# Kernel tuning notes

Hardware: AMD Instinct MI355X
Metric: run time of the kernel (lower is better)

## Reference

```python
import jax, jax.numpy as jnp
import numpy as np

NEG_INF = -1.0e9  # matches torch masked_fill value

def setup_inputs() -> dict:
    key = jax.random.key(0)
    kq, kk, kv, km = jax.random.split(key, 4)
    B, S, D = 16, 2048, 128
    query = jax.random.normal(kq, (B, S, D), dtype=jnp.float32)
    k = jax.random.normal(kk, (B, S, D), dtype=jnp.float32)
    value = jax.random.normal(kv, (B, S, D), dtype=jnp.float32)
    mask = jax.random.randint(km, (B, S, S), 0, 2).astype(jnp.bool_)
    return {"query": query, "key": k, "value": value, "mask": mask}

def reference(query, key, value, mask):
    # scores: [B, Sq, Sk]
    D = key.shape[-1]
    scale = jnp.sqrt(jnp.asarray(D, dtype=query.dtype))
    scores = jnp.einsum('bqd,bkd->bqk', query, key) / scale
    scores = jnp.where(mask, jnp.asarray(NEG_INF, dtype=scores.dtype), scores)
    attn = jax.nn.softmax(scores, axis=2)
    # dropout p=0.0 -> identity in eval/reference
    out = jnp.einsum('bqk,bkd->bqd', attn, value)
    return out, attn
```

## Files before the change

kernel.cpp:

```cpp
#include <hip/hip_runtime.h>

#define S 2048
#define Dh 128
#define NB 16
#define OUT_ELEMS ((size_t)NB * S * Dh)
#define NEG_BIG -1.0e9f
#define SCALE 0.08838834764831845f

typedef __attribute__((ext_vector_type(8))) short bf16x8;
typedef __attribute__((ext_vector_type(4))) float f32x4;
typedef __attribute__((ext_vector_type(4))) short s16x4;

__device__ __forceinline__ short f2bf(float x) {
    unsigned u = __float_as_uint(x);
    u += 0x7fffu + ((u >> 16) & 1u);
    return (short)(u >> 16);
}

__device__ __forceinline__ s16x4 pack4(float4 v) {
    s16x4 r;
    r.x = f2bf(v.x); r.y = f2bf(v.y); r.z = f2bf(v.z); r.w = f2bf(v.w);
    return r;
}

__global__ void detect_mask(const unsigned char* __restrict__ m, int* __restrict__ flag) {
    __shared__ int any;
    if (threadIdx.x == 0) any = 0;
    __syncthreads();
    int t = threadIdx.x;
    unsigned char v = (unsigned char)(m[t * 4 + 1] | m[t * 4 + 2] | m[t * 4 + 3]);
    if (v) atomicOr(&any, 1);
    __syncthreads();
    if (t == 0) *flag = any;
}

__global__ __launch_bounds__(256) void transpose_v(const float* __restrict__ V,
                                                   short* __restrict__ Vt) {
    const int kb = blockIdx.x, b = blockIdx.y;
    const float* Vb = V + ((size_t)b * S + kb * 64) * Dh;
    short* VtB = Vt + (size_t)b * Dh * S;
    __shared__ float Ls[64][132];
    const int t = threadIdx.x;
#pragma unroll
    for (int i = 0; i < 8; i++) {
        int idx = t + i * 256;
        int r = idx >> 5, c = (idx & 31) << 2;
        *(float4*)&Ls[r][c] = *(const float4*)(Vb + r * Dh + c);
    }
    __syncthreads();
#pragma unroll
    for (int i = 0; i < 8; i++) {
        int idx = t + i * 256;
        int n = idx >> 4, kc = (idx & 15) << 2;
        s16x4 o;
        o.x = f2bf(Ls[kc + 0][n]);
        o.y = f2bf(Ls[kc + 1][n]);
        o.z = f2bf(Ls[kc + 2][n]);
        o.w = f2bf(Ls[kc + 3][n]);
        *(s16x4*)(VtB + (size_t)n * S + kb * 64 + kc) = o;
    }
}

__global__ __launch_bounds__(256) void cvt_bf16(const float* __restrict__ in,
                                                short* __restrict__ out) {
    const size_t n4 = (size_t)NB * S * Dh / 4;
    for (size_t i = (size_t)blockIdx.x * 256 + threadIdx.x; i < n4; i += (size_t)gridDim.x * 256) {
        float4 v = ((const float4*)in)[i];
        ((s16x4*)out)[i] = pack4(v);
    }
}

__global__ __launch_bounds__(256, 2) void qk_stats(const short* __restrict__ Qbf,
                                                   const short* __restrict__ Kbf,
                                                   const void* __restrict__ maskp,
                                                   const int* __restrict__ flagp,
                                                   float2* __restrict__ part) {
    const int kt = blockIdx.x, qt = blockIdx.y, b = blockIdx.z;
    const short* Qb = Qbf + ((size_t)b * S + qt * 128) * Dh;
    const short* Kb = Kbf + ((size_t)b * S + kt * 128) * Dh;
    __shared__ short As[128][72];
    __shared__ short Bs[128][72];
    __shared__ __align__(16) unsigned char Ms[128][144];
    const int t = threadIdx.x;
    const int w = t >> 6, lane = t & 63, fr = lane & 15, quad = lane >> 4;
    const int mw = (w >> 1) * 64, nw = (w & 1) * 64;
    f32x4 acc[4][4] = {};

    const int flag = *flagp;
    if (flag) {
        const unsigned char* Mb = (const unsigned char*)maskp + ((size_t)b * S + qt * 128) * S + (size_t)kt * 128;
#pragma unroll
        for (int i = 0; i < 4; i++) {
            int idx = t + i * 256;
            int r = idx >> 3, c = (idx & 7) * 16;
            *(int4*)&Ms[r][c] = *(const int4*)(Mb + (size_t)r * S + c);
        }
    } else {
        const int* Mb = (const int*)maskp + ((size_t)b * S + qt * 128) * S + (size_t)kt * 128;
#pragma unroll
        for (int i = 0; i < 16; i++) {
            int idx = t + i * 256;
            int r = idx >> 5, c = (idx & 31) * 4;
            int4 m = *(const int4*)(Mb + (size_t)r * S + c);
            uchar4 o;
            o.x = (unsigned char)(m.x != 0);
            o.y = (unsigned char)(m.y != 0);
            o.z = (unsigned char)(m.z != 0);
            o.w = (unsigned char)(m.w != 0);
            *(uchar4*)&Ms[r][c] = o;
        }
    }

    for (int k0 = 0; k0 < Dh; k0 += 64) {
        __syncthreads();
#pragma unroll
        for (int i = 0; i < 4; i++) {
            int idx = t + i * 256;
            int r = idx >> 3, c8 = (idx & 7) * 8;
            *(bf16x8*)&As[r][c8] = *(const bf16x8*)(Qb + (size_t)r * Dh + k0 + c8);
            *(bf16x8*)&Bs[r][c8] = *(const bf16x8*)(Kb + (size_t)r * Dh + k0 + c8);
        }
        __syncthreads();
#pragma unroll
        for (int kc = 0; kc < 2; kc++) {
            const int ko = kc * 32 + quad * 8;
            bf16x8 af[4], bf[4];
#pragma unroll
            for (int mi = 0; mi < 4; mi++) af[mi] = *(const bf16x8*)&As[mw + mi * 16 + fr][ko];
#pragma unroll
            for (int ni = 0; ni < 4; ni++) bf[ni] = *(const bf16x8*)&Bs[nw + ni * 16 + fr][ko];
#pragma unroll
            for (int mi = 0; mi < 4; mi++)
#pragma unroll
                for (int ni = 0; ni < 4; ni++)
                    acc[mi][ni] = __builtin_amdgcn_mfma_f32_16x16x32_bf16(af[mi], bf[ni], acc[mi][ni], 0, 0, 0);
        }
    }

    __syncthreads();
    float2* pm = (float2*)&As[0][0];
#pragma unroll
    for (int mi = 0; mi < 4; mi++)
#pragma unroll
        for (int r = 0; r < 4; r++) {
            const int lrow = mw + mi * 16 + quad * 4 + r;
            float s[4];
#pragma unroll
            for (int ni = 0; ni < 4; ni++) {
                const int lcol = nw + ni * 16 + fr;
                float v = acc[mi][ni][r] * SCALE;
                if (Ms[lrow][lcol]) v = NEG_BIG;
                s[ni] = v;
            }
            float mx = fmaxf(fmaxf(s[0], s[1]), fmaxf(s[2], s[3]));
#pragma unroll
            for (int o = 8; o > 0; o >>= 1) mx = fmaxf(mx, __shfl_xor(mx, o, 64));
            float l = __expf(s[0] - mx) + __expf(s[1] - mx) +
                      __expf(s[2] - mx) + __expf(s[3] - mx);
#pragma unroll
            for (int o = 8; o > 0; o >>= 1) l += __shfl_xor(l, o, 64);
            if (fr == 0) pm[lrow * 2 + (w & 1)] = make_float2(mx, l);
        }

    __syncthreads();
    if (t < 128) {
        float2 a = pm[t * 2 + 0], c = pm[t * 2 + 1];
        float M = fmaxf(a.x, c.x);
        float L = a.y * __expf(a.x - M) + c.y * __expf(c.x - M);
        part[((size_t)(b * 16 + kt)) * S + qt * 128 + t] = make_float2(M, L);
    }
}

__global__ __launch_bounds__(256) void reduce_stats(const float2* __restrict__ part,
                                                    float2* __restrict__ stats) {
    const int rid = blockIdx.x * 256 + threadIdx.x;
    const int b = rid >> 11, row = rid & (S - 1);
    float2 p[16];
    float M = -3.4e38f;
#pragma unroll
    for (int kt = 0; kt < 16; kt++) {
        p[kt] = part[((size_t)(b * 16 + kt)) * S + row];
        M = fmaxf(M, p[kt].x);
    }
    float L = 0.f;
#pragma unroll
    for (int kt = 0; kt < 16; kt++) L += p[kt].y * __expf(p[kt].x - M);
    stats[rid] = make_float2(M, 1.0f / L);
}

__global__ __launch_bounds__(256, 2) void fused_pv(const short* __restrict__ Qbf,
                                                   const short* __restrict__ Kbf,
                                                   const short* __restrict__ Vt,
                                                   const void* __restrict__ maskp,
                                                   const int* __restrict__ flagp,
                                                   const float2* __restrict__ stats,
                                                   float* __restrict__ Attn,
                                                   float* __restrict__ Out) {
    const int qt = blockIdx.x, b = blockIdx.y;
    const short* QbfB = Qbf + ((size_t)b * S + qt * 64) * Dh;
    const short* KbfB = Kbf + (size_t)b * S * Dh;
    const short* VtB  = Vt  + (size_t)b * Dh * S;
    float* AttnB = Attn + ((size_t)b * S + qt * 64) * S;
    float* OutB  = Out  + ((size_t)b * S + qt * 64) * Dh;
    const int flag = *flagp;

    __shared__ short Qs[2][64][72];
    __shared__ short Ks[2][128][72];
    __shared__ short Ps[2][64][72];
    unsigned char (*Ms)[128] = (unsigned char (*)[128]) &Ps[0][0][0];

    const int t = threadIdx.x, w = t >> 6, lane = t & 63, fr = lane & 15, quad = lane >> 4;
    const int mo = (w >> 1) * 32, no = (w & 1) * 64;

#pragma unroll
    for (int i = 0; i < 4; i++) {
        int idx = t + i * 256;
        int r = idx >> 4, c8 = (idx & 15) * 8;
        *(bf16x8*)&Qs[c8 >> 6][r][c8 & 63] = *(const bf16x8*)(QbfB + (size_t)r * Dh + c8);
    }

    float2 st[2][4];
#pragma unroll
    for (int mi = 0; mi < 2; mi++)
#pragma unroll
        for (int r = 0; r < 4; r++)
            st[mi][r] = stats[(size_t)b * S + qt * 64 + mo + mi * 16 + quad * 4 + r];

    f32x4 acc_o[2][4] = {};

    bf16x8 kv[8];
    int4 mreg[2];
#pragma unroll
    for (int i = 0; i < 8; i++) {
        int idx = t + i * 256;
        int r = idx >> 4, c8 = (idx & 15) * 8;
        kv[i] = *(const bf16x8*)(KbfB + (size_t)r * Dh + c8);
    }
    if (flag) {
        const unsigned char* Mb = (const unsigned char*)maskp + ((size_t)b * S + qt * 64) * S;
#pragma unroll
        for (int i = 0; i < 2; i++) {
            int idx = t + i * 256;
            int r = idx >> 3, c16 = (idx & 7) * 16;
            mreg[i] = *(const int4*)(Mb + (size_t)r * S + c16);
        }
    }

    for (int kt = 0; kt < 16; kt++) {
        __syncthreads();
#pragma unroll
        for (int i = 0; i < 8; i++) {
            int idx = t + i * 256;
            int r = idx >> 4, c8 = (idx & 15) * 8;
            *(bf16x8*)&Ks[c8 >> 6][r][c8 & 63] = kv[i];
        }
        if (flag) {
#pragma unroll
            for (int i = 0; i < 2; i++) {
                int idx = t + i * 256;
                int r = idx >> 3, c16 = (idx & 7) * 16;
                *(int4*)&Ms[r][c16] = mreg[i];
            }
        } else {
            const int* Mb = (const int*)maskp + ((size_t)b * S + qt * 64) * S + (size_t)kt * 128;
#pragma unroll
            for (int i = 0; i < 8; i++) {
                int idx = t + i * 256;
                int r = idx >> 5, c4 = (idx & 31) * 4;
                int4 m = *(const int4*)(Mb + (size_t)r * S + c4);
                uchar4 o;
                o.x = (unsigned char)(m.x != 0);
                o.y = (unsigned char)(m.y != 0);
                o.z = (unsigned char)(m.z != 0);
                o.w = (unsigned char)(m.w != 0);
                *(uchar4*)&Ms[r][c4] = o;
            }
        }
        __syncthreads();

        if (kt < 15) {
#pragma unroll
            for (int i = 0; i < 8; i++) {
                int idx = t + i * 256;
                int r = idx >> 4, c8 = (idx & 15) * 8;
                kv[i] = *(const bf16x8*)(KbfB + (size_t)((kt + 1) * 128 + r) * Dh + c8);
            }
            if (flag) {
                const unsigned char* Mb = (const unsigned char*)maskp + ((size_t)b * S + qt * 64) * S + (size_t)(kt + 1) * 128;
#pragma unroll
                for (int i = 0; i < 2; i++) {
                    int idx = t + i * 256;
                    int r = idx >> 3, c16 = (idx & 7) * 16;
                    mreg[i] = *(const int4*)(Mb + (size_t)r * S + c16);
                }
            }
        }

        f32x4 acc_s[2][4] = {};
#pragma unroll
        for (int ks = 0; ks < 4; ks++) {
            const int h = ks >> 1, o = (ks & 1) * 32 + quad * 8;
            bf16x8 af[2], bf[4];
#pragma unroll
            for (int mi = 0; mi < 2; mi++) af[mi] = *(const bf16x8*)&Qs[h][mo + mi * 16 + fr][o];
#pragma unroll
            for (int ni = 0; ni < 4; ni++) bf[ni] = *(const bf16x8*)&Ks[h][no + ni * 16 + fr][o];
#pragma unroll
            for (int mi = 0; mi < 2; mi++)
#pragma unroll
                for (int ni = 0; ni < 4; ni++)
                    acc_s[mi][ni] = __builtin_amdgcn_mfma_f32_16x16x32_bf16(af[mi], bf[ni], acc_s[mi][ni], 0, 0, 0);
        }

        short ps[2][4][4];
#pragma unroll
        for (int mi = 0; mi < 2; mi++)
#pragma unroll
            for (int ni = 0; ni < 4; ni++)
#pragma unroll
                for (int r = 0; r < 4; r++) {
                    const int row = mo + mi * 16 + quad * 4 + r;
                    const int col = no + ni * 16 + fr;
                    float v = acc_s[mi][ni][r] * SCALE;
                    if (Ms[row][col]) v = NEG_BIG;
                    float p = __expf(v - st[mi][r].x) * st[mi][r].y;
                    AttnB[(size_t)row * S + kt * 128 + col] = p;
                    ps[mi][ni][r] = f2bf(p);
                }
        __syncthreads();
#pragma unroll
        for (int mi = 0; mi < 2; mi++)
#pragma unroll
            for (int ni = 0; ni < 4; ni++)
#pragma unroll
                for (int r = 0; r < 4; r++) {
                    const int row = mo + mi * 16 + quad * 4 + r;
                    const int col = no + ni * 16 + fr;
                    Ps[col >> 6][row][col & 63] = ps[mi][ni][r];
                }
        __syncthreads();

#pragma unroll
        for (int ks = 0; ks < 4; ks++) {
            const int h = ks >> 1, o = (ks & 1) * 32 + quad * 8;
            bf16x8 paf[2], pbf[4];
#pragma unroll
            for (int mi = 0; mi < 2; mi++) paf[mi] = *(const bf16x8*)&Ps[h][mo + mi * 16 + fr][o];
#pragma unroll
            for (int ni = 0; ni < 4; ni++)
                pbf[ni] = *(const bf16x8*)(VtB + (size_t)(no + ni * 16 + fr) * S + kt * 128 + ks * 32 + quad * 8);
#pragma unroll
            for (int mi = 0; mi < 2; mi++)
#pragma unroll
                for (int ni = 0; ni < 4; ni++)
                    acc_o[mi][ni] = __builtin_amdgcn_mfma_f32_16x16x32_bf16(paf[mi], pbf[ni], acc_o[mi][ni], 0, 0, 0);
        }
    }

#pragma unroll
    for (int mi = 0; mi < 2; mi++)
#pragma unroll
        for (int ni = 0; ni < 4; ni++)
#pragma unroll
            for (int r = 0; r < 4; r++) {
                const int row = mo + mi * 16 + quad * 4 + r;
                const int col = no + ni * 16 + fr;
                OutB[(size_t)row * Dh + col] = acc_o[mi][ni][r];
            }
}

__global__ __launch_bounds__(256, 2) void qk_kernel(const float* __restrict__ Q,
                                                    const float* __restrict__ Km,
                                                    float* __restrict__ Sc,
                                                    const void* __restrict__ maskp,
                                                    const int* __restrict__ flagp,
                                                    float2* __restrict__ part,
                                                    const int fuse) {
    const int kt = blockIdx.x, qt = blockIdx.y, b = blockIdx.z;
    const float* Qb = Q + ((size_t)b * S + qt * 128) * Dh;
    const float* Kb = Km + ((size_t)b * S + kt * 128) * Dh;
    __shared__ short As[128][72];
    __shared__ short Bs[128][72];
    __shared__ __align__(16) unsigned char Ms[128][144];
    const int t = threadIdx.x;
    const int w = t >> 6, lane = t & 63, fr = lane & 15, quad = lane >> 4;
    const int mw = (w >> 1) * 64, nw = (w & 1) * 64;
    f32x4 acc[4][4] = {};

    if (fuse) {
        const int flag = *flagp;
        if (flag) {
            const unsigned char* Mb = (const unsigned char*)maskp + ((size_t)b * S + qt * 128) * S + (size_t)kt * 128;
#pragma unroll
            for (int i = 0; i < 4; i++) {
                int idx = t + i * 256;
                int r = idx >> 3, c = (idx & 7) * 16;
                *(int4*)&Ms[r][c] = *(const int4*)(Mb + (size_t)r * S + c);
            }
        } else {
            const int* Mb = (const int*)maskp + ((size_t)b * S + qt * 128) * S + (size_t)kt * 128;
#pragma unroll
            for (int i = 0; i < 16; i++) {
                int idx = t + i * 256;
                int r = idx >> 5, c = (idx & 31) * 4;
                int4 m = *(const int4*)(Mb + (size_t)r * S + c);
                uchar4 o;
                o.x = (unsigned char)(m.x != 0);
                o.y = (unsigned char)(m.y != 0);
                o.z = (unsigned char)(m.z != 0);
                o.w = (unsigned char)(m.w != 0);
                *(uchar4*)&Ms[r][c] = o;
            }
        }
    }

    for (int k0 = 0; k0 < Dh; k0 += 64) {
        __syncthreads();
#pragma unroll
        for (int i = 0; i < 8; i++) {
            int idx = t + i * 256;
            int r = idx >> 4, c = (idx & 15) << 2;
            float4 qv = *(const float4*)(Qb + r * Dh + k0 + c);
            float4 kv = *(const float4*)(Kb + r * Dh + k0 + c);
            *(s16x4*)&As[r][c] = pack4(qv);
            *(s16x4*)&Bs[r][c] = pack4(kv);
        }
        __syncthreads();
#pragma unroll
        for (int kc = 0; kc < 2; kc++) {
            const int ko = kc * 32 + quad * 8;
            bf16x8 af[4], bf[4];
#pragma unroll
            for (int mi = 0; mi < 4; mi++) af[mi] = *(const bf16x8*)&As[mw + mi * 16 + fr][ko];
#pragma unroll
            for (int ni = 0; ni < 4; ni++) bf[ni] = *(const bf16x8*)&Bs[nw + ni * 16 + fr][ko];
#pragma unroll
            for (int mi = 0; mi < 4; mi++)
#pragma unroll
                for (int ni = 0; ni < 4; ni++)
                    acc[mi][ni] = __builtin_amdgcn_mfma_f32_16x16x32_bf16(af[mi], bf[ni], acc[mi][ni], 0, 0, 0);
        }
    }

    __syncthreads();
    float2* pm = (float2*)&As[0][0];
    float* ScB = Sc + (size_t)b * S * S;
#pragma unroll
    for (int mi = 0; mi < 4; mi++)
#pragma unroll
        for (int r = 0; r < 4; r++) {
            const int lrow = mw + mi * 16 + quad * 4 + r;
            const size_t grow = (size_t)(qt * 128 + lrow);
            float s[4];
#pragma unroll
            for (int ni = 0; ni < 4; ni++) {
                const int lcol = nw + ni * 16 + fr;
                float v = acc[mi][ni][r] * SCALE;
                if (fuse && Ms[lrow][lcol]) v = NEG_BIG;
                s[ni] = v;
                ScB[grow * S + kt * 128 + lcol] = v;
            }
            if (fuse) {
                float mx = fmaxf(fmaxf(s[0], s[1]), fmaxf(s[2], s[3]));
#pragma unroll
                for (int o = 8; o > 0; o >>= 1) mx = fmaxf(mx, __shfl_xor(mx, o, 64));
                float l = __expf(s[0] - mx) + __expf(s[1] - mx) +
                          __expf(s[2] - mx) + __expf(s[3] - mx);
#pragma unroll
                for (int o = 8; o > 0; o >>= 1) l += __shfl_xor(l, o, 64);
                if (fr == 0) pm[lrow * 2 + (w & 1)] = make_float2(mx, l);
            }
        }

    if (fuse) {
        __syncthreads();
        if (t < 128) {
            float2 a = pm[t * 2 + 0], c = pm[t * 2 + 1];
            float M = fmaxf(a.x, c.x);
            float L = a.y * __expf(a.x - M) + c.y * __expf(c.x - M);
            part[((size_t)(b * 16 + kt)) * S + qt * 128 + t] = make_float2(M, L);
        }
    }
}

__global__ __launch_bounds__(256) void softmax_kernel(float* __restrict__ Sc,
                                                      const void* __restrict__ maskp,
                                                      const int* __restrict__ flagp) {
    const int b = blockIdx.y;
    const int w = threadIdx.x >> 6, lane = threadIdx.x & 63;
    const int row = blockIdx.x * 4 + w;
    float* R = Sc + ((size_t)b * S + row) * S;
    float4* R4 = (float4*)R;
    const int flag = flagp ? *flagp : 0;

    float sv[32];
    if (flag) {
        const uchar4* M4 = (const uchar4*)((const unsigned char*)maskp + ((size_t)b * S + row) * S);
#pragma unroll
        for (int j = 0; j < 8; j++) {
            float4 v = R4[lane + 64 * j];
            uchar4 m = M4[lane + 64 * j];
            sv[4 * j + 0] = m.x ? NEG_BIG : v.x;
            sv[4 * j + 1] = m.y ? NEG_BIG : v.y;
            sv[4 * j + 2] = m.z ? NEG_BIG : v.z;
            sv[4 * j + 3] = m.w ? NEG_BIG : v.w;
        }
    } else {
        const int4* M4 = (const int4*)((const int*)maskp + ((size_t)b * S + row) * S);
#pragma unroll
        for (int j = 0; j < 8; j++) {
            float4 v = R4[lane + 64 * j];
            int4 m = M4[lane + 64 * j];
            sv[4 * j + 0] = m.x ? NEG_BIG : v.x;
            sv[4 * j + 1] = m.y ? NEG_BIG : v.y;
            sv[4 * j + 2] = m.z ? NEG_BIG : v.z;
            sv[4 * j + 3] = m.w ? NEG_BIG : v.w;
        }
    }

    float mx = sv[0];
#pragma unroll
    for (int i = 1; i < 32; i++) mx = fmaxf(mx, sv[i]);
    for (int o = 32; o > 0; o >>= 1) mx = fmaxf(mx, __shfl_xor(mx, o, 64));

    float sum = 0.f;
#pragma unroll
    for (int i = 0; i < 32; i++) {
        sv[i] = __expf(sv[i] - mx);
        sum += sv[i];
    }
    for (int o = 32; o > 0; o >>= 1) sum += __shfl_xor(sum, o, 64);
    const float inv = 1.0f / sum;

#pragma unroll
    for (int j = 0; j < 8; j++) {
        float4 p;
        p.x = sv[4 * j + 0] * inv;
        p.y = sv[4 * j + 1] * inv;
        p.z = sv[4 * j + 2] * inv;
        p.w = sv[4 * j + 3] * inv;
        R4[lane + 64 * j] = p;
    }
}

__global__ __launch_bounds__(256, 2) void pv_kernel(float* __restrict__ Sc,
                                                    const float* __restrict__ V,
                                                    const short* __restrict__ Vt,
                                                    const int useVt,
                                                    float* __restrict__ Out,
                                                    const float2* __restrict__ stats,
                                                    const int fuse) {
    const int mt = blockIdx.x, b = blockIdx.y;
    float* ScB = Sc + (size_t)b * S * S + (size_t)mt * 64 * S;
    const float* Vb = V + (size_t)b * S * Dh;
    const short* VtB = Vt + (size_t)b * Dh * S;
    float* OutB = Out + ((size_t)b * S + mt * 64) * Dh;
    __shared__ short As[64][72];
    __shared__ float2 sstat[64];
    const int t = threadIdx.x, w = t >> 6, lane = t & 63, fr = lane & 15, quad = lane >> 4;
    const int mw = (w >> 1) * 32, nw = (w & 1) * 64;
    f32x4 acc[2][4] = {};

    if (fuse && t < 64) sstat[t] = stats[(size_t)b * S + mt * 64 + t];

    for (int k0 = 0; k0 < S; k0 += 64) {
        __syncthreads();
#pragma unroll
        for (int i = 0; i < 4; i++) {
            int idx = t + i * 256;
            int r = idx >> 4, c = (idx & 15) << 2;
            float4 v = *(const float4*)(ScB + (size_t)r * S + k0 + c);
            if (fuse) {
                float2 stv = sstat[r];
                v.x = __expf(v.x - stv.x) * stv.y;
                v.y = __expf(v.y - stv.x) * stv.y;
                v.z = __expf(v.z - stv.x) * stv.y;
                v.w = __expf(v.w - stv.x) * stv.y;
                *(float4*)(ScB + (size_t)r * S + k0 + c) = v;
            }
            *(s16x4*)&As[r][c] = pack4(v);
        }
        __syncthreads();
#pragma unroll
        for (int kc = 0; kc < 2; kc++) {
            const int ko = kc * 32 + quad * 8;
            bf16x8 af[2], bf[4];
#pragma unroll
            for (int mi = 0; mi < 2; mi++) af[mi] = *(const bf16x8*)&As[mw + mi * 16 + fr][ko];
            if (useVt) {
#pragma unroll
                for (int ni = 0; ni < 4; ni++)
                    bf[ni] = *(const bf16x8*)(VtB + (size_t)(nw + ni * 16 + fr) * S + k0 + ko);
            } else {
#pragma unroll
                for (int ni = 0; ni < 4; ni++) {
                    int n = nw + ni * 16 + fr;
#pragma unroll
                    for (int j = 0; j < 8; j++) bf[ni][j] = f2bf(Vb[(size_t)(k0 + ko + j) * Dh + n]);
                }
            }
#pragma unroll
            for (int mi = 0; mi < 2; mi++)
#pragma unroll
                for (int ni = 0; ni < 4; ni++)
                    acc[mi][ni] = __builtin_amdgcn_mfma_f32_16x16x32_bf16(af[mi], bf[ni], acc[mi][ni], 0, 0, 0);
        }
    }

#pragma unroll
    for (int mi = 0; mi < 2; mi++)
#pragma unroll
        for (int ni = 0; ni < 4; ni++)
#pragma unroll
            for (int r = 0; r < 4; r++) {
                int row = mw + mi * 16 + quad * 4 + r;
                int col = nw + ni * 16 + fr;
                OutB[(size_t)row * Dh + col] = acc[mi][ni][r];
            }
}

extern "C" void kernel_launch(void* const* d_in, const int* in_sizes, int n_in,
                              void* d_out, int out_size, void* d_ws, size_t ws_size,
                              hipStream_t stream) {
    const float* Q = (const float*)d_in[0];
    const float* Km = (const float*)d_in[1];
    const float* V = (const float*)d_in[2];
    const void* M = d_in[3];
    float* out = (float*)d_out;
    float* attn = out + OUT_ELEMS;

    const size_t VT_BYTES   = (size_t)NB * Dh * S * sizeof(short);
    const size_t QBF_BYTES  = (size_t)NB * S * Dh * sizeof(short);
    const size_t KBF_BYTES  = QBF_BYTES;
    const size_t STATS_BYTES = (size_t)NB * S * sizeof(float2);
    const size_t REQ_NEW = VT_BYTES + QBF_BYTES + KBF_BYTES + STATS_BYTES + 64;

    float2* part = (float2*)d_out;

    if (ws_size >= REQ_NEW) {
        short* Vt   = (short*)d_ws;
        short* Qbf  = (short*)((char*)d_ws + VT_BYTES);
        short* Kbf  = (short*)((char*)d_ws + VT_BYTES + QBF_BYTES);
        float2* stats = (float2*)((char*)d_ws + VT_BYTES + QBF_BYTES + KBF_BYTES);
        int* flag = (int*)((char*)d_ws + VT_BYTES + QBF_BYTES + KBF_BYTES + STATS_BYTES);

        detect_mask<<<1, 256, 0, stream>>>((const unsigned char*)M, flag);
        transpose_v<<<dim3(32, NB), 256, 0, stream>>>(V, Vt);
        cvt_bf16<<<2048, 256, 0, stream>>>(Q, Qbf);
        cvt_bf16<<<2048, 256, 0, stream>>>(Km, Kbf);
        qk_stats<<<dim3(16, 16, NB), 256, 0, stream>>>(Qbf, Kbf, M, flag, part);
        reduce_stats<<<dim3((NB * S) / 256), 256, 0, stream>>>(part, stats);
        fused_pv<<<dim3(32, NB), 256, 0, stream>>>(Qbf, Kbf, Vt, M, flag, stats, attn, out);
        return;
    }

    int useVt = 0, fuse = 0;
    short* Vt = nullptr;
    float2* stats = nullptr;
    int* flag = nullptr;

    if (ws_size >= VT_BYTES + STATS_BYTES + 64) {
        useVt = 1; fuse = 1;
        Vt = (short*)d_ws;
        stats = (float2*)((char*)d_ws + VT_BYTES);
        flag = (int*)((char*)d_ws + VT_BYTES + STATS_BYTES);
    } else if (ws_size >= VT_BYTES + 64) {
        useVt = 1;
        Vt = (short*)d_ws;
        flag = (int*)((char*)d_ws + VT_BYTES);
    } else if (ws_size >= 64) {
        flag = (int*)d_ws;
    }

    if (flag) detect_mask<<<1, 256, 0, stream>>>((const unsigned char*)M, flag);
    if (useVt) transpose_v<<<dim3(32, NB), 256, 0, stream>>>(V, Vt);

    qk_kernel<<<dim3(16, 16, NB), 256, 0, stream>>>(Q, Km, attn, M, flag, part, fuse);

    if (fuse) {
        reduce_stats<<<dim3((NB * S) / 256), 256, 0, stream>>>(part, stats);
        pv_kernel<<<dim3(32, NB), 256, 0, stream>>>(attn, V, Vt, useVt, out, stats, 1);
    } else {
        softmax_kernel<<<dim3(512, NB), 256, 0, stream>>>(attn, M, flag);
        pv_kernel<<<dim3(32, NB), 256, 0, stream>>>(attn, V, Vt, useVt, out, nullptr, 0);
    }
}
```

Before: 691.5 us.

## Restructure attention into online-softmax flash PV pass plus separate attn-write pass

```diff
diff --git a/kernel.cpp b/kernel.cpp
--- a/kernel.cpp
+++ b/kernel.cpp
@@ -70,12 +70,199 @@
     }
 }
 
-__global__ __launch_bounds__(256, 2) void qk_stats(const short* __restrict__ Qbf,
+__global__ __launch_bounds__(256, 2) void flash_pv(const short* __restrict__ Qbf,
                                                    const short* __restrict__ Kbf,
+                                                   const short* __restrict__ Vt,
                                                    const void* __restrict__ maskp,
                                                    const int* __restrict__ flagp,
-                                                   float2* __restrict__ part) {
-    const int kt = blockIdx.x, qt = blockIdx.y, b = blockIdx.z;
+                                                   float2* __restrict__ stats,
+                                                   float* __restrict__ Out) {
+    const int bid = blockIdx.x;
+    const int xcd = bid & 7, kk = bid >> 3;
+    const int b = xcd * 2 + (kk >> 5), qt = kk & 31;
+
+    const short* QbfB = Qbf + ((size_t)b * S + qt * 64) * Dh;
+    const short* KbfB = Kbf + (size_t)b * S * Dh;
+    const short* VtB  = Vt  + (size_t)b * Dh * S;
+    float* OutB = Out + ((size_t)b * S + qt * 64) * Dh;
+    const int flag = *flagp;
+
+    __shared__ short Qs[2][64][72];
+    __shared__ short Ks[2][128][72];
+    __shared__ short Ps[2][64][72];
+    __shared__ __align__(16) unsigned char Msk[64][128];
+
+    const int t = threadIdx.x, w = t >> 6, lane = t & 63, fr = lane & 15, quad = lane >> 4;
+    const int mo = w * 16;
+
+#pragma unroll
+    for (int i = 0; i < 4; i++) {
+        int idx = t + i * 256;
+        int r = idx >> 4, c8 = (idx & 15) * 8;
+        *(bf16x8*)&Qs[c8 >> 6][r][c8 & 63] = *(const bf16x8*)(QbfB + (size_t)r * Dh + c8);
+    }
+
+    float m[4], l[4];
+#pragma unroll
+    for (int r = 0; r < 4; r++) { m[r] = -3.4e38f; l[r] = 0.f; }
+    f32x4 acc_o[8] = {};
+
+    bf16x8 kv[8];
+    int4 mreg[2];
+#pragma unroll
+    for (int i = 0; i < 8; i++) {
+        int idx = t + i * 256;
+        int r = idx >> 4, c8 = (idx & 15) * 8;
+        kv[i] = *(const bf16x8*)(KbfB + (size_t)r * Dh + c8);
+    }
+    if (flag) {
+        const unsigned char* Mb = (const unsigned char*)maskp + ((size_t)b * S + qt * 64) * S;
+#pragma unroll
+        for (int i = 0; i < 2; i++) {
+            int idx = t + i * 256;
+            int r = idx >> 3, c16 = (idx & 7) * 16;
+            mreg[i] = *(const int4*)(Mb + (size_t)r * S + c16);
+        }
+    }
+
+    for (int kt = 0; kt < 16; kt++) {
+        __syncthreads();
+#pragma unroll
+        for (int i = 0; i < 8; i++) {
+            int idx = t + i * 256;
+            int r = idx >> 4, c8 = (idx & 15) * 8;
+            *(bf16x8*)&Ks[c8 >> 6][r][c8 & 63] = kv[i];
+        }
+        if (flag) {
+#pragma unroll
+            for (int i = 0; i < 2; i++) {
+                int idx = t + i * 256;
+                int r = idx >> 3, c16 = (idx & 7) * 16;
+                *(int4*)&Msk[r][c16] = mreg[i];
+            }
+        } else {
+            const int* Mb = (const int*)maskp + ((size_t)b * S + qt * 64) * S + (size_t)kt * 128;
+#pragma unroll
+            for (int i = 0; i < 8; i++) {
+                int idx = t + i * 256;
+                int r = idx >> 5, c4 = (idx & 31) * 4;
+                int4 mv = *(const int4*)(Mb + (size_t)r * S + c4);
+                uchar4 o;
+                o.x = (unsigned char)(mv.x != 0);
+                o.y = (unsigned char)(mv.y != 0);
+                o.z = (unsigned char)(mv.z != 0);
+                o.w = (unsigned char)(mv.w != 0);
+                *(uchar4*)&Msk[r][c4] = o;
+            }
+        }
+        __syncthreads();
+
+        if (kt < 15) {
+#pragma unroll
+            for (int i = 0; i < 8; i++) {
+                int idx = t + i * 256;
+                int r = idx >> 4, c8 = (idx & 15) * 8;
+                kv[i] = *(const bf16x8*)(KbfB + (size_t)((kt + 1) * 128 + r) * Dh + c8);
+            }
+            if (flag) {
+                const unsigned char* Mb = (const unsigned char*)maskp + ((size_t)b * S + qt * 64) * S + (size_t)(kt + 1) * 128;
+#pragma unroll
+                for (int i = 0; i < 2; i++) {
+                    int idx = t + i * 256;
+                    int r = idx >> 3, c16 = (idx & 7) * 16;
+                    mreg[i] = *(const int4*)(Mb + (size_t)r * S + c16);
+                }
+            }
+        }
+
+        f32x4 acc_s[8] = {};
+#pragma unroll
+        for (int ks = 0; ks < 4; ks++) {
+            const int h = ks >> 1, o = (ks & 1) * 32 + quad * 8;
+            bf16x8 af = *(const bf16x8*)&Qs[h][mo + fr][o];
+            bf16x8 bfv[8];
+#pragma unroll
+            for (int ni = 0; ni < 8; ni++) bfv[ni] = *(const bf16x8*)&Ks[h][ni * 16 + fr][o];
+#pragma unroll
+            for (int ni = 0; ni < 8; ni++)
+                acc_s[ni] = __builtin_amdgcn_mfma_f32_16x16x32_bf16(af, bfv[ni], acc_s[ni], 0, 0, 0);
+        }
+
+#pragma unroll
+        for (int r = 0; r < 4; r++) {
+            const int row = mo + quad * 4 + r;
+            float s[8];
+#pragma unroll
+            for (int ni = 0; ni < 8; ni++) {
+                float v = acc_s[ni][r] * SCALE;
+                if (Msk[row][ni * 16 + fr]) v = NEG_BIG;
+                s[ni] = v;
+            }
+            float mx = s[0];
+#pragma unroll
+            for (int ni = 1; ni < 8; ni++) mx = fmaxf(mx, s[ni]);
+#pragma unroll
+            for (int o = 8; o > 0; o >>= 1) mx = fmaxf(mx, __shfl_xor(mx, o, 64));
+            const float mn = fmaxf(m[r], mx);
+            const float f = __expf(m[r] - mn);
+            float p[8], lt = 0.f;
+#pragma unroll
+            for (int ni = 0; ni < 8; ni++) { p[ni] = __expf(s[ni] - mn); lt += p[ni]; }
+#pragma unroll
+            for (int o = 8; o > 0; o >>= 1) lt += __shfl_xor(lt, o, 64);
+            l[r] = l[r] * f + lt;
+            m[r] = mn;
+#pragma unroll
+            for (int ni = 0; ni < 8; ni++) acc_o[ni][r] *= f;
+#pragma unroll
+            for (int ni = 0; ni < 8; ni++) {
+                const int col = ni * 16 + fr;
+                Ps[col >> 6][row][col & 63] = f2bf(p[ni]);
+            }
+        }
+        __syncthreads();
+
+#pragma unroll
+        for (int ks = 0; ks < 4; ks++) {
+            const int h = ks >> 1, o = (ks & 1) * 32 + quad * 8;
+            bf16x8 paf = *(const bf16x8*)&Ps[h][mo + fr][o];
+            bf16x8 pb[8];
+#pragma unroll
+            for (int ni = 0; ni < 8; ni++)
+                pb[ni] = *(const bf16x8*)(VtB + (size_t)(ni * 16 + fr) * S + kt * 128 + ks * 32 + quad * 8);
+#pragma unroll
+            for (int ni = 0; ni < 8; ni++)
+                acc_o[ni] = __builtin_amdgcn_mfma_f32_16x16x32_bf16(paf, pb[ni], acc_o[ni], 0, 0, 0);
+        }
+    }
+
+    float invl[4];
+#pragma unroll
+    for (int r = 0; r < 4; r++) invl[r] = 1.0f / l[r];
+#pragma unroll
+    for (int ni = 0; ni < 8; ni++)
+#pragma unroll
+        for (int r = 0; r < 4; r++) {
+            const int row = mo + quad * 4 + r;
+            OutB[(size_t)row * Dh + ni * 16 + fr] = acc_o[ni][r] * invl[r];
+        }
+    if (fr == 0) {
+#pragma unroll
+        for (int r = 0; r < 4; r++)
+            stats[(size_t)b * S + qt * 64 + mo + quad * 4 + r] = make_float2(m[r], invl[r]);
+    }
+}
+
+__global__ __launch_bounds__(256, 2) void attn_write(const short* __restrict__ Qbf,
+                                                     const short* __restrict__ Kbf,
+                                                     const void* __restrict__ maskp,
+                                                     const int* __restrict__ flagp,
+                                                     const float2* __restrict__ stats,
+                                                     float* __restrict__ Attn) {
+    const int bid = blockIdx.x;
+    const int xcd = bid & 7, kk = bid >> 3;
+    const int b = xcd * 2 + (kk >> 8), rem = kk & 255, qt = rem >> 4, kt = rem & 15;
+
     const short* Qb = Qbf + ((size_t)b * S + qt * 128) * Dh;
     const short* Kb = Kbf + ((size_t)b * S + kt * 128) * Dh;
     __shared__ short As[128][72];
@@ -101,15 +288,22 @@
         for (int i = 0; i < 16; i++) {
             int idx = t + i * 256;
             int r = idx >> 5, c = (idx & 31) * 4;
-            int4 m = *(const int4*)(Mb + (size_t)r * S + c);
+            int4 mv = *(const int4*)(Mb + (size_t)r * S + c);
             uchar4 o;
-            o.x = (unsigned char)(m.x != 0);
-            o.y = (unsigned char)(m.y != 0);
-            o.z = (unsigned char)(m.z != 0);
-            o.w = (unsigned char)(m.w != 0);
+            o.x = (unsigned char)(mv.x != 0);
+            o.y = (unsigned char)(mv.y != 0);
+            o.z = (unsigned char)(mv.z != 0);
+            o.w = (unsigned char)(mv.w != 0);
             *(uchar4*)&Ms[r][c] = o;
         }
     }
+
+    float2 st[4][4];
+#pragma unroll
+    for (int mi = 0; mi < 4; mi++)
+#pragma unroll
+        for (int r = 0; r < 4; r++)
+            st[mi][r] = stats[(size_t)b * S + qt * 128 + mw + mi * 16 + quad * 4 + r];
 
     for (int k0 = 0; k0 < Dh; k0 += 64) {
         __syncthreads();
@@ -137,38 +331,20 @@
         }
     }
 
-    __syncthreads();
-    float2* pm = (float2*)&As[0][0];
+    float* AttnB = Attn + (size_t)b * S * S;
 #pragma unroll
     for (int mi = 0; mi < 4; mi++)
 #pragma unroll
-        for (int r = 0; r < 4; r++) {
-            const int lrow = mw + mi * 16 + quad * 4 + r;
-            float s[4];
-#pragma unroll
-            for (int ni = 0; ni < 4; ni++) {
+        for (int ni = 0; ni < 4; ni++)
+#pragma unroll
+            for (int r = 0; r < 4; r++) {
+                const int lrow = mw + mi * 16 + quad * 4 + r;
                 const int lcol = nw + ni * 16 + fr;
                 float v = acc[mi][ni][r] * SCALE;
                 if (Ms[lrow][lcol]) v = NEG_BIG;
-                s[ni] = v;
-            }
-            float mx = fmaxf(fmaxf(s[0], s[1]), fmaxf(s[2], s[3]));
-#pragma unroll
-            for (int o = 8; o > 0; o >>= 1) mx = fmaxf(mx, __shfl_xor(mx, o, 64));
-            float l = __expf(s[0] - mx) + __expf(s[1] - mx) +
-                      __expf(s[2] - mx) + __expf(s[3] - mx);
-#pragma unroll
-            for (int o = 8; o > 0; o >>= 1) l += __shfl_xor(l, o, 64);
-            if (fr == 0) pm[lrow * 2 + (w & 1)] = make_float2(mx, l);
-        }
-
-    __syncthreads();
-    if (t < 128) {
-        float2 a = pm[t * 2 + 0], c = pm[t * 2 + 1];
-        float M = fmaxf(a.x, c.x);
-        float L = a.y * __expf(a.x - M) + c.y * __expf(c.x - M);
-        part[((size_t)(b * 16 + kt)) * S + qt * 128 + t] = make_float2(M, L);
-    }
+                const float p = __expf(v - st[mi][r].x) * st[mi][r].y;
+                AttnB[(size_t)(qt * 128 + lrow) * S + kt * 128 + lcol] = p;
+            }
 }
 
 __global__ __launch_bounds__(256) void reduce_stats(const float2* __restrict__ part,
@@ -186,187 +362,6 @@
 #pragma unroll
     for (int kt = 0; kt < 16; kt++) L += p[kt].y * __expf(p[kt].x - M);
     stats[rid] = make_float2(M, 1.0f / L);
-}
-
-__global__ __launch_bounds__(256, 2) void fused_pv(const short* __restrict__ Qbf,
-                                                   const short* __restrict__ Kbf,
-                                                   const short* __restrict__ Vt,
-                                                   const void* __restrict__ maskp,
-                                                   const int* __restrict__ flagp,
-                                                   const float2* __restrict__ stats,
-                                                   float* __restrict__ Attn,
-                                                   float* __restrict__ Out) {
-    const int qt = blockIdx.x, b = blockIdx.y;
-    const short* QbfB = Qbf + ((size_t)b * S + qt * 64) * Dh;
-    const short* KbfB = Kbf + (size_t)b * S * Dh;
-    const short* VtB  = Vt  + (size_t)b * Dh * S;
-    float* AttnB = Attn + ((size_t)b * S + qt * 64) * S;
-    float* OutB  = Out  + ((size_t)b * S + qt * 64) * Dh;
-    const int flag = *flagp;
-
-    __shared__ short Qs[2][64][72];
-    __shared__ short Ks[2][128][72];
-    __shared__ short Ps[2][64][72];
-    unsigned char (*Ms)[128] = (unsigned char (*)[128]) &Ps[0][0][0];
-
-    const int t = threadIdx.x, w = t >> 6, lane = t & 63, fr = lane & 15, quad = lane >> 4;
-    const int mo = (w >> 1) * 32, no = (w & 1) * 64;
-
-#pragma unroll
-    for (int i = 0; i < 4; i++) {
-        int idx = t + i * 256;
-        int r = idx >> 4, c8 = (idx & 15) * 8;
-        *(bf16x8*)&Qs[c8 >> 6][r][c8 & 63] = *(const bf16x8*)(QbfB + (size_t)r * Dh + c8);
-    }
-
-    float2 st[2][4];
-#pragma unroll
-    for (int mi = 0; mi < 2; mi++)
-#pragma unroll
-        for (int r = 0; r < 4; r++)
-            st[mi][r] = stats[(size_t)b * S + qt * 64 + mo + mi * 16 + quad * 4 + r];
-
-    f32x4 acc_o[2][4] = {};
-
-    bf16x8 kv[8];
-    int4 mreg[2];
-#pragma unroll
-    for (int i = 0; i < 8; i++) {
-        int idx = t + i * 256;
-        int r = idx >> 4, c8 = (idx & 15) * 8;
-        kv[i] = *(const bf16x8*)(KbfB + (size_t)r * Dh + c8);
-    }
-    if (flag) {
-        const unsigned char* Mb = (const unsigned char*)maskp + ((size_t)b * S + qt * 64) * S;
-#pragma unroll
-        for (int i = 0; i < 2; i++) {
-            int idx = t + i * 256;
-            int r = idx >> 3, c16 = (idx & 7) * 16;
-            mreg[i] = *(const int4*)(Mb + (size_t)r * S + c16);
-        }
-    }
-
-    for (int kt = 0; kt < 16; kt++) {
-        __syncthreads();
-#pragma unroll
-        for (int i = 0; i < 8; i++) {
-            int idx = t + i * 256;
-            int r = idx >> 4, c8 = (idx & 15) * 8;
-            *(bf16x8*)&Ks[c8 >> 6][r][c8 & 63] = kv[i];
-        }
-        if (flag) {
-#pragma unroll
-            for (int i = 0; i < 2; i++) {
-                int idx = t + i * 256;
-                int r = idx >> 3, c16 = (idx & 7) * 16;
-                *(int4*)&Ms[r][c16] = mreg[i];
-            }
-        } else {
-            const int* Mb = (const int*)maskp + ((size_t)b * S + qt * 64) * S + (size_t)kt * 128;
-#pragma unroll
-            for (int i = 0; i < 8; i++) {
-                int idx = t + i * 256;
-                int r = idx >> 5, c4 = (idx & 31) * 4;
-                int4 m = *(const int4*)(Mb + (size_t)r * S + c4);
-                uchar4 o;
-                o.x = (unsigned char)(m.x != 0);
-                o.y = (unsigned char)(m.y != 0);
-                o.z = (unsigned char)(m.z != 0);
-                o.w = (unsigned char)(m.w != 0);
-                *(uchar4*)&Ms[r][c4] = o;
-            }
-        }
-        __syncthreads();
-
-        if (kt < 15) {
-#pragma unroll
-            for (int i = 0; i < 8; i++) {
-                int idx = t + i * 256;
-                int r = idx >> 4, c8 = (idx & 15) * 8;
-                kv[i] = *(const bf16x8*)(KbfB + (size_t)((kt + 1) * 128 + r) * Dh + c8);
-            }
-            if (flag) {
-                const unsigned char* Mb = (const unsigned char*)maskp + ((size_t)b * S + qt * 64) * S + (size_t)(kt + 1) * 128;
-#pragma unroll
-                for (int i = 0; i < 2; i++) {
-                    int idx = t + i * 256;
-                    int r = idx >> 3, c16 = (idx & 7) * 16;
-                    mreg[i] = *(const int4*)(Mb + (size_t)r * S + c16);
-                }
-            }
-        }
-
-        f32x4 acc_s[2][4] = {};
-#pragma unroll
-        for (int ks = 0; ks < 4; ks++) {
-            const int h = ks >> 1, o = (ks & 1) * 32 + quad * 8;
-            bf16x8 af[2], bf[4];
-#pragma unroll
-            for (int mi = 0; mi < 2; mi++) af[mi] = *(const bf16x8*)&Qs[h][mo + mi * 16 + fr][o];
-#pragma unroll
-            for (int ni = 0; ni < 4; ni++) bf[ni] = *(const bf16x8*)&Ks[h][no + ni * 16 + fr][o];
-#pragma unroll
-            for (int mi = 0; mi < 2; mi++)
-#pragma unroll
-                for (int ni = 0; ni < 4; ni++)
-                    acc_s[mi][ni] = __builtin_amdgcn_mfma_f32_16x16x32_bf16(af[mi], bf[ni], acc_s[mi][ni], 0, 0, 0);
-        }
-
-        short ps[2][4][4];
-#pragma unroll
-        for (int mi = 0; mi < 2; mi++)
-#pragma unroll
-            for (int ni = 0; ni < 4; ni++)
-#pragma unroll
-                for (int r = 0; r < 4; r++) {
-                    const int row = mo + mi * 16 + quad * 4 + r;
-                    const int col = no + ni * 16 + fr;
-                    float v = acc_s[mi][ni][r] * SCALE;
-                    if (Ms[row][col]) v = NEG_BIG;
-                    float p = __expf(v - st[mi][r].x) * st[mi][r].y;
-                    AttnB[(size_t)row * S + kt * 128 + col] = p;
-                    ps[mi][ni][r] = f2bf(p);
-                }
-        __syncthreads();
-#pragma unroll
-        for (int mi = 0; mi < 2; mi++)
-#pragma unroll
-            for (int ni = 0; ni < 4; ni++)
-#pragma unroll
-                for (int r = 0; r < 4; r++) {
-                    const int row = mo + mi * 16 + quad * 4 + r;
-                    const int col = no + ni * 16 + fr;
-                    Ps[col >> 6][row][col & 63] = ps[mi][ni][r];
-                }
-        __syncthreads();
-
-#pragma unroll
-        for (int ks = 0; ks < 4; ks++) {
-            const int h = ks >> 1, o = (ks & 1) * 32 + quad * 8;
-            bf16x8 paf[2], pbf[4];
-#pragma unroll
-            for (int mi = 0; mi < 2; mi++) paf[mi] = *(const bf16x8*)&Ps[h][mo + mi * 16 + fr][o];
-#pragma unroll
-            for (int ni = 0; ni < 4; ni++)
-                pbf[ni] = *(const bf16x8*)(VtB + (size_t)(no + ni * 16 + fr) * S + kt * 128 + ks * 32 + quad * 8);
-#pragma unroll
-            for (int mi = 0; mi < 2; mi++)
-#pragma unroll
-                for (int ni = 0; ni < 4; ni++)
-                    acc_o[mi][ni] = __builtin_amdgcn_mfma_f32_16x16x32_bf16(paf[mi], pbf[ni], acc_o[mi][ni], 0, 0, 0);
-        }
-    }
-
-#pragma unroll
-    for (int mi = 0; mi < 2; mi++)
-#pragma unroll
-        for (int ni = 0; ni < 4; ni++)
-#pragma unroll
-            for (int r = 0; r < 4; r++) {
-                const int row = mo + mi * 16 + quad * 4 + r;
-                const int col = no + ni * 16 + fr;
-                OutB[(size_t)row * Dh + col] = acc_o[mi][ni][r];
-            }
 }
 
 __global__ __launch_bounds__(256, 2) void qk_kernel(const float* __restrict__ Q,
@@ -403,12 +398,12 @@
             for (int i = 0; i < 16; i++) {
                 int idx = t + i * 256;
                 int r = idx >> 5, c = (idx & 31) * 4;
-                int4 m = *(const int4*)(Mb + (size_t)r * S + c);
+                int4 mv = *(const int4*)(Mb + (size_t)r * S + c);
                 uchar4 o;
-                o.x = (unsigned char)(m.x != 0);
-                o.y = (unsigned char)(m.y != 0);
-                o.z = (unsigned char)(m.z != 0);
-                o.w = (unsigned char)(m.w != 0);
+                o.x = (unsigned char)(mv.x != 0);
+                o.y = (unsigned char)(mv.y != 0);
+                o.z = (unsigned char)(mv.z != 0);
+                o.w = (unsigned char)(mv.w != 0);
                 *(uchar4*)&Ms[r][c] = o;
             }
         }
@@ -464,11 +459,11 @@
                 float mx = fmaxf(fmaxf(s[0], s[1]), fmaxf(s[2], s[3]));
 #pragma unroll
                 for (int o = 8; o > 0; o >>= 1) mx = fmaxf(mx, __shfl_xor(mx, o, 64));
-                float l = __expf(s[0] - mx) + __expf(s[1] - mx) +
-                          __expf(s[2] - mx) + __expf(s[3] - mx);
-#pragma unroll
-                for (int o = 8; o > 0; o >>= 1) l += __shfl_xor(l, o, 64);
-                if (fr == 0) pm[lrow * 2 + (w & 1)] = make_float2(mx, l);
+                float lsum = __expf(s[0] - mx) + __expf(s[1] - mx) +
+                             __expf(s[2] - mx) + __expf(s[3] - mx);
+#pragma unroll
+                for (int o = 8; o > 0; o >>= 1) lsum += __shfl_xor(lsum, o, 64);
+                if (fr == 0) pm[lrow * 2 + (w & 1)] = make_float2(mx, lsum);
             }
         }
 
@@ -499,22 +494,22 @@
 #pragma unroll
         for (int j = 0; j < 8; j++) {
             float4 v = R4[lane + 64 * j];
-            uchar4 m = M4[lane + 64 * j];
-            sv[4 * j + 0] = m.x ? NEG_BIG : v.x;
-            sv[4 * j + 1] = m.y ? NEG_BIG : v.y;
-            sv[4 * j + 2] = m.z ? NEG_BIG : v.z;
-            sv[4 * j + 3] = m.w ? NEG_BIG : v.w;
+            uchar4 mv = M4[lane + 64 * j];
+            sv[4 * j + 0] = mv.x ? NEG_BIG : v.x;
+            sv[4 * j + 1] = mv.y ? NEG_BIG : v.y;
+            sv[4 * j + 2] = mv.z ? NEG_BIG : v.z;
+            sv[4 * j + 3] = mv.w ? NEG_BIG : v.w;
         }
     } else {
         const int4* M4 = (const int4*)((const int*)maskp + ((size_t)b * S + row) * S);
 #pragma unroll
         for (int j = 0; j < 8; j++) {
             float4 v = R4[lane + 64 * j];
-            int4 m = M4[lane + 64 * j];
-            sv[4 * j + 0] = m.x ? NEG_BIG : v.x;
-            sv[4 * j + 1] = m.y ? NEG_BIG : v.y;
-            sv[4 * j + 2] = m.z ? NEG_BIG : v.z;
-            sv[4 * j + 3] = m.w ? NEG_BIG : v.w;
+            int4 mv = M4[lane + 64 * j];
+            sv[4 * j + 0] = mv.x ? NEG_BIG : v.x;
+            sv[4 * j + 1] = mv.y ? NEG_BIG : v.y;
+            sv[4 * j + 2] = mv.z ? NEG_BIG : v.z;
+            sv[4 * j + 3] = mv.w ? NEG_BIG : v.w;
         }
     }
 
@@ -635,8 +630,6 @@
     const size_t STATS_BYTES = (size_t)NB * S * sizeof(float2);
     const size_t REQ_NEW = VT_BYTES + QBF_BYTES + KBF_BYTES + STATS_BYTES + 64;
 
-    float2* part = (float2*)d_out;
-
     if (ws_size >= REQ_NEW) {
         short* Vt   = (short*)d_ws;
         short* Qbf  = (short*)((char*)d_ws + VT_BYTES);
@@ -648,12 +641,12 @@
         transpose_v<<<dim3(32, NB), 256, 0, stream>>>(V, Vt);
         cvt_bf16<<<2048, 256, 0, stream>>>(Q, Qbf);
         cvt_bf16<<<2048, 256, 0, stream>>>(Km, Kbf);
-        qk_stats<<<dim3(16, 16, NB), 256, 0, stream>>>(Qbf, Kbf, M, flag, part);
-        reduce_stats<<<dim3((NB * S) / 256), 256, 0, stream>>>(part, stats);
-        fused_pv<<<dim3(32, NB), 256, 0, stream>>>(Qbf, Kbf, Vt, M, flag, stats, attn, out);
+        flash_pv<<<512, 256, 0, stream>>>(Qbf, Kbf, Vt, M, flag, stats, out);
+        attn_write<<<4096, 256, 0, stream>>>(Qbf, Kbf, M, flag, stats, attn);
         return;
     }
 
+    float2* part = (float2*)d_out;
     int useVt = 0, fuse = 0;
     short* Vt = nullptr;
     float2* stats = nullptr;
```

After: 656.3 us. -5.1%, faster.
